# Kernel optimization log

Measured on AMD Instinct MI355X. Metric: run time of the kernel, lower is better.

The kernel has to match this reference:

```python
import jax, jax.numpy as jnp
import numpy as np

B, S, E = 2, 2048, 2048
H, KVH = 16, 4
HD = E // H          # 128
REP = H // KVH       # 4
THETA = 100000.0


def _rope_cos_sin(seqlen, head_dim, theta=THETA):
    # Faithful to precompute_pos_cis: exponent is arange(0, d, 2) (NOT divided by d)
    freqs = 1.0 / theta ** jnp.arange(0, head_dim, 2, dtype=jnp.float32)[: head_dim // 2]
    ang = jnp.outer(jnp.arange(seqlen, dtype=jnp.float32), freqs)  # (S, HD/2)
    return jnp.cos(ang), jnp.sin(ang)


def _apply_rotary(t, cos, sin):
    # t: (B, S, h, HD) -> complex pairs along last dim
    b, s, h, d = t.shape
    t = t.astype(jnp.float32).reshape(b, s, h, d // 2, 2)
    tr, ti = t[..., 0], t[..., 1]
    c = cos[None, :, None, :]
    sn = sin[None, :, None, :]
    out_r = tr * c - ti * sn
    out_i = tr * sn + ti * c
    return jnp.stack([out_r, out_i], axis=-1).reshape(b, s, h, d)


def setup_inputs() -> dict:
    key = jax.random.key(0)
    ks = jax.random.split(key, 9)
    sc_e = 1.0 / np.sqrt(E)
    return {
        "x": jax.random.normal(ks[0], (B, S, E), jnp.float32),
        "wq": jax.random.normal(ks[1], (E, H * HD), jnp.float32) * sc_e,
        "bq": jax.random.normal(ks[2], (H * HD,), jnp.float32) * 0.01,
        "wk": jax.random.normal(ks[3], (E, KVH * HD), jnp.float32) * sc_e,
        "bk": jax.random.normal(ks[4], (KVH * HD,), jnp.float32) * 0.01,
        "wv": jax.random.normal(ks[5], (E, KVH * HD), jnp.float32) * sc_e,
        "bv": jax.random.normal(ks[6], (KVH * HD,), jnp.float32) * 0.01,
        "wo": jax.random.normal(ks[7], (H * HD, E), jnp.float32) * sc_e,
        "bo": jax.random.normal(ks[8], (E,), jnp.float32) * 0.01,
    }


def reference(x, wq, bq, wk, bk, wv, bv, wo, bo):
    b, s, _ = x.shape
    xq = (x @ wq + bq).reshape(b, s, H, HD)
    xk = (x @ wk + bk).reshape(b, s, KVH, HD)
    xv = (x @ wv + bv).reshape(b, s, KVH, HD)

    cos, sin = _rope_cos_sin(s, HD)
    xq = _apply_rotary(xq, cos, sin)
    xk = _apply_rotary(xk, cos, sin)

    # GQA: group query heads over shared KV heads instead of materializing repeat_kv
    q = xq.transpose(0, 2, 1, 3).reshape(b, KVH, REP, s, HD)  # (B, G, R, S, D)
    k = xk.transpose(0, 2, 1, 3)                               # (B, G, S, D)
    v = xv.astype(jnp.float32).transpose(0, 2, 1, 3)           # (B, G, S, D)

    scores = jnp.einsum("bgrqd,bgkd->bgrqk", q, k) / jnp.sqrt(jnp.float32(HD))
    causal = jnp.tril(jnp.ones((s, s), dtype=bool))
    scores = jnp.where(causal[None, None, None], scores, jnp.float32(-jnp.inf))
    attn = jax.nn.softmax(scores, axis=-1)
    out = jnp.einsum("bgrqk,bgkd->bgrqd", attn, v)  # (B, G, R, S, D)
    out = out.reshape(b, H, s, HD).transpose(0, 2, 1, 3).reshape(b, s, H * HD)
    return out @ wo + bo
```

## Files before the change

### kernel.cpp

```cpp
#include <hip/hip_runtime.h>
#include <math.h>

#define BB 2
#define SS 2048
#define EE 2048
#define HH 16
#define KVH 4
#define HD 128

typedef __attribute__((ext_vector_type(8))) short short8;
typedef __attribute__((ext_vector_type(4))) float f32x4;

__device__ __forceinline__ short f2b(float f) {
  unsigned u = __float_as_uint(f);
  unsigned r = (u + 0x7fffu + ((u >> 16) & 1u)) >> 16;
  return (short)r;
}

__device__ __forceinline__ void async_load16(const void* g, void* l) {
  __builtin_amdgcn_global_load_lds(
      (const __attribute__((address_space(1))) void*)g,
      (__attribute__((address_space(3))) void*)l, 16, 0, 0);
}

__device__ __forceinline__ float rope_freq(int jp) {
  return exp2f(-(float)(2 * jp) * 16.609640474436812f);
}

__global__ void f32_to_bf16(const float* __restrict__ in, short* __restrict__ out) {
  int i = (blockIdx.x * 256 + threadIdx.x) * 8;
  float4 a = *(const float4*)(in + i);
  float4 b = *(const float4*)(in + i + 4);
  short8 c;
  c[0] = f2b(a.x); c[1] = f2b(a.y); c[2] = f2b(a.z); c[3] = f2b(a.w);
  c[4] = f2b(b.x); c[5] = f2b(b.y); c[6] = f2b(b.z); c[7] = f2b(b.w);
  *(short8*)(out + i) = c;
}

__global__ void transpose_f2b(const float* __restrict__ in, short* __restrict__ out,
                              int K, int N) {
  __shared__ short tile[32][33];
  int n0 = blockIdx.x * 32, k0 = blockIdx.y * 32;
  int tx = threadIdx.x, ty = threadIdx.y;
#pragma unroll
  for (int i = 0; i < 32; i += 8)
    tile[ty + i][tx] = f2b(in[(size_t)(k0 + ty + i) * N + n0 + tx]);
  __syncthreads();
#pragma unroll
  for (int i = 0; i < 32; i += 8)
    out[(size_t)(n0 + ty + i) * K + k0 + tx] = tile[tx][ty + i];
}

__global__ __launch_bounds__(256) void gemm_qkv(
    const short* __restrict__ A, const short* __restrict__ Bt,
    const float* __restrict__ bq, const float* __restrict__ bk,
    const float* __restrict__ bv,
    short* __restrict__ qbuf, short* __restrict__ kbuf, short* __restrict__ vtr) {
  __shared__ __align__(16) short Sm[128 * 136];
  short* Al = Sm;
  short* Bl = Sm + 128 * 64;
  const int K = EE;
  int t = threadIdx.x, lane = t & 63, w = t >> 6;
  int wm = (w >> 1) * 64, wn = (w & 1) * 64;
  int id = blockIdx.y * 32 + blockIdx.x;
  int swz = (id & 7) * 96 + (id >> 3);
  int m0 = (swz & 31) * 128, n0 = (swz >> 5) * 128;
  const short* Ab = A + (size_t)m0 * K;
  const short* Bb = Bt + (size_t)n0 * K;
  int srow = t >> 3, scol = (t & 7) * 8;
  int lj = lane & 15, lr = lane >> 4;
  f32x4 acc[4][4] = {};
  for (int k0 = 0; k0 < K; k0 += 64) {
#pragma unroll
    for (int q = 0; q < 4; q++) {
      async_load16(Ab + (size_t)(q * 32 + srow) * K + k0 + scol,
                   (char*)Al + q * 4096 + w * 1024);
      async_load16(Bb + (size_t)(q * 32 + srow) * K + k0 + scol,
                   (char*)Bl + q * 4096 + w * 1024);
    }
    __syncthreads();
    short8 a0[4], a1[4], b0[4], b1[4];
#pragma unroll
    for (int i = 0; i < 4; i++) {
      a0[i] = *(const short8*)&Al[(wm + i * 16 + lj) * 64 + lr * 8];
      a1[i] = *(const short8*)&Al[(wm + i * 16 + lj) * 64 + 32 + lr * 8];
    }
#pragma unroll
    for (int j = 0; j < 4; j++) {
      b0[j] = *(const short8*)&Bl[(wn + j * 16 + lj) * 64 + lr * 8];
      b1[j] = *(const short8*)&Bl[(wn + j * 16 + lj) * 64 + 32 + lr * 8];
    }
#pragma unroll
    for (int i = 0; i < 4; i++)
#pragma unroll
      for (int j = 0; j < 4; j++) {
        acc[i][j] = __builtin_amdgcn_mfma_f32_16x16x32_bf16(a0[i], b0[j], acc[i][j], 0, 0, 0);
        acc[i][j] = __builtin_amdgcn_mfma_f32_16x16x32_bf16(a1[i], b1[j], acc[i][j], 0, 0, 0);
      }
    __syncthreads();
  }
  if (n0 < 2048) {
#pragma unroll
    for (int j = 0; j < 4; j++) {
      int d = wn + j * 16 + lj;
      float bias = bq[n0 + d];
      float freq = rope_freq(d >> 1);
      bool odd = (d & 1) != 0;
#pragma unroll
      for (int i = 0; i < 4; i++)
#pragma unroll
        for (int r = 0; r < 4; r++) {
          int mloc = wm + i * 16 + lr * 4 + r;
          int s = (m0 + mloc) & (SS - 1);
          float val = acc[i][j][r] + bias;
          float other = __shfl_xor(val, 1, 64);
          float ang = (float)s * freq;
          float cs = cosf(ang), sn = sinf(ang);
          float res = odd ? (other * sn + val * cs) : (val * cs - other * sn);
          Sm[mloc * 136 + d] = f2b(res);
        }
    }
  } else if (n0 < 2560) {
    int base = n0 - 2048;
#pragma unroll
    for (int j = 0; j < 4; j++) {
      int d = wn + j * 16 + lj;
      float bias = bk[base + d];
      float freq = rope_freq(d >> 1);
      bool odd = (d & 1) != 0;
#pragma unroll
      for (int i = 0; i < 4; i++)
#pragma unroll
        for (int r = 0; r < 4; r++) {
          int mloc = wm + i * 16 + lr * 4 + r;
          int s = (m0 + mloc) & (SS - 1);
          float val = acc[i][j][r] + bias;
          float other = __shfl_xor(val, 1, 64);
          float ang = (float)s * freq;
          float cs = cosf(ang), sn = sinf(ang);
          float res = odd ? (other * sn + val * cs) : (val * cs - other * sn);
          Sm[mloc * 136 + d] = f2b(res);
        }
    }
  } else {
    int base = n0 - 2560;
#pragma unroll
    for (int j = 0; j < 4; j++) {
      int d = wn + j * 16 + lj;
      float bias = bv[base + d];
#pragma unroll
      for (int i = 0; i < 4; i++)
#pragma unroll
        for (int r = 0; r < 4; r++) {
          int mloc = wm + i * 16 + lr * 4 + r;
          Sm[d * 136 + mloc] = f2b(acc[i][j][r] + bias);
        }
    }
  }
  __syncthreads();
  int r0 = t >> 4, ch = t & 15;
  if (n0 < 2048) {
#pragma unroll
    for (int p = 0; p < 8; p++) {
      int row = p * 16 + r0;
      *(short8*)(qbuf + (size_t)(m0 + row) * 2048 + n0 + ch * 8) =
          *(const short8*)&Sm[row * 136 + ch * 8];
    }
  } else if (n0 < 2560) {
    int kvh = (n0 - 2048) >> 7;
    int b = m0 >> 11, s0 = m0 & (SS - 1);
    short* dst = kbuf + ((size_t)(b * KVH + kvh) * SS + s0) * HD;
#pragma unroll
    for (int p = 0; p < 8; p++) {
      int row = p * 16 + r0;
      *(short8*)(dst + (size_t)row * HD + ch * 8) = *(const short8*)&Sm[row * 136 + ch * 8];
    }
  } else {
    int kvh = (n0 - 2560) >> 7;
    int b = m0 >> 11, s0 = m0 & (SS - 1);
    short* dst = vtr + ((size_t)(b * KVH + kvh) * HD) * SS + s0;
#pragma unroll
    for (int p = 0; p < 8; p++) {
      int row = p * 16 + r0;
      *(short8*)(dst + (size_t)row * SS + ch * 8) = *(const short8*)&Sm[row * 136 + ch * 8];
    }
  }
}

__global__ __launch_bounds__(256) void attn_kernel(
    const short* __restrict__ qb, const short* __restrict__ kb,
    const short* __restrict__ vt, short* __restrict__ ao) {
  __shared__ __align__(16) short Kl[64 * 128];
  __shared__ __align__(16) short Vl[128 * 64];
  __shared__ __align__(16) short Pl[4 * 16 * 64];
  int t = threadIdx.x, lane = t & 63, w = t >> 6;
  int lj = lane & 15, lr = lane >> 4;
  int id = blockIdx.x + (blockIdx.y << 5) + (blockIdx.z << 9);
  int swz = (id & 7) * 128 + (id >> 3);
  int qt = swz & 31, h = (swz >> 5) & 15, b = swz >> 9;
  int kvh = h >> 2;
  int qb0 = qt * 64;
  const short* qbase = qb + (size_t)(b * SS) * 2048 + h * HD;
  const short* kbase = kb + (size_t)(b * KVH + kvh) * SS * HD;
  const short* vbase = vt + (size_t)(b * KVH + kvh) * HD * SS;
  short8 aq[4];
  int sq = qb0 + w * 16 + lj;
#pragma unroll
  for (int kk = 0; kk < 4; kk++)
    aq[kk] = *(const short8*)(qbase + (size_t)sq * 2048 + kk * 32 + lr * 8);
  f32x4 O[8] = {};
  const float NEG = -1e30f;
  float mrow[4] = {NEG, NEG, NEG, NEG};
  float lrow[4] = {0.f, 0.f, 0.f, 0.f};
  const float scale = 0.088388347648318447f;
  int nkt = qt + 1;
  for (int kt = 0; kt < nkt; ++kt) {
    short8 gk[4], gv[4];
#pragma unroll
    for (int i = 0; i < 4; i++) {
      gk[i] = *(const short8*)(kbase + (size_t)(kt * 64 + i * 16 + (t >> 4)) * HD + (t & 15) * 8);
      gv[i] = *(const short8*)(vbase + (size_t)(i * 32 + (t >> 3)) * SS + kt * 64 + (t & 7) * 8);
    }
#pragma unroll
    for (int i = 0; i < 4; i++) {
      *(short8*)&Kl[(i * 16 + (t >> 4)) * 128 + (t & 15) * 8] = gk[i];
      *(short8*)&Vl[(i * 32 + (t >> 3)) * 64 + (t & 7) * 8] = gv[i];
    }
    __syncthreads();
    f32x4 S[4];
#pragma unroll
    for (int nt = 0; nt < 4; nt++) {
      f32x4 sc = {};
#pragma unroll
      for (int kk = 0; kk < 4; kk++) {
        short8 bk_ = *(const short8*)&Kl[(nt * 16 + lj) * 128 + kk * 32 + lr * 8];
        sc = __builtin_amdgcn_mfma_f32_16x16x32_bf16(aq[kk], bk_, sc, 0, 0, 0);
      }
      S[nt] = sc;
    }
    int rowg = qb0 + w * 16 + lr * 4;
#pragma unroll
    for (int nt = 0; nt < 4; nt++) {
      int colg = kt * 64 + nt * 16 + lj;
#pragma unroll
      for (int r = 0; r < 4; r++) {
        float v = S[nt][r] * scale;
        if (colg > rowg + r) v = NEG;
        S[nt][r] = v;
      }
    }
    float alpha[4];
#pragma unroll
    for (int r = 0; r < 4; r++) {
      float m_ = fmaxf(fmaxf(S[0][r], S[1][r]), fmaxf(S[2][r], S[3][r]));
#pragma unroll
      for (int off = 1; off < 16; off <<= 1) m_ = fmaxf(m_, __shfl_xor(m_, off, 64));
      float mn = fmaxf(mrow[r], m_);
      alpha[r] = __expf(mrow[r] - mn);
      mrow[r] = mn;
    }
    float ls[4] = {0.f, 0.f, 0.f, 0.f};
#pragma unroll
    for (int nt = 0; nt < 4; nt++)
#pragma unroll
      for (int r = 0; r < 4; r++) {
        float p = __expf(S[nt][r] - mrow[r]);
        ls[r] += p;
        Pl[(w * 16 + lr * 4 + r) * 64 + nt * 16 + lj] = f2b(p);
      }
#pragma unroll
    for (int r = 0; r < 4; r++) {
      float s_ = ls[r];
#pragma unroll
      for (int off = 1; off < 16; off <<= 1) s_ += __shfl_xor(s_, off, 64);
      lrow[r] = lrow[r] * alpha[r] + s_;
    }
#pragma unroll
    for (int jt = 0; jt < 8; jt++)
#pragma unroll
      for (int r = 0; r < 4; r++) O[jt][r] *= alpha[r];
#pragma unroll
    for (int kk = 0; kk < 2; kk++) {
      short8 ap = *(const short8*)&Pl[(w * 16 + lj) * 64 + kk * 32 + lr * 8];
#pragma unroll
      for (int jt = 0; jt < 8; jt++) {
        short8 bv_ = *(const short8*)&Vl[(jt * 16 + lj) * 64 + kk * 32 + lr * 8];
        O[jt] = __builtin_amdgcn_mfma_f32_16x16x32_bf16(ap, bv_, O[jt], 0, 0, 0);
      }
    }
    __syncthreads();
  }
  size_t obase = (size_t)(b * SS + qb0 + w * 16) * 2048 + h * HD;
#pragma unroll
  for (int jt = 0; jt < 8; jt++)
#pragma unroll
    for (int r = 0; r < 4; r++) {
      int row = lr * 4 + r;
      ao[obase + (size_t)row * 2048 + jt * 16 + lj] = f2b(O[jt][r] / lrow[r]);
    }
}

__global__ __launch_bounds__(256) void gemm_out(
    const short* __restrict__ A, const short* __restrict__ Bt,
    const float* __restrict__ bo, float* __restrict__ out) {
  __shared__ __align__(16) short Al[128 * 32];
  __shared__ __align__(16) short Bl[128 * 32];
  const int K = EE;
  int t = threadIdx.x, lane = t & 63, w = t >> 6;
  int wm = (w >> 1) * 64, wn = (w & 1) * 64;
  int id = blockIdx.y * 32 + blockIdx.x;
  int swz = (id & 7) * 64 + (id >> 3);
  int m0 = (swz & 31) * 128, n0 = (swz >> 5) * 128;
  const short* Ab = A + (size_t)m0 * K;
  const short* Bb = Bt + (size_t)n0 * K;
  int sr = t >> 2, sc = (t & 3) * 8;
  char* AlB = (char*)Al + w * 1024;
  char* BlB = (char*)Bl + w * 1024;
  f32x4 acc[4][4] = {};
  for (int k0 = 0; k0 < K; k0 += 32) {
    async_load16(Ab + (size_t)sr * K + k0 + sc, AlB);
    async_load16(Ab + (size_t)(64 + sr) * K + k0 + sc, AlB + 4096);
    async_load16(Bb + (size_t)sr * K + k0 + sc, BlB);
    async_load16(Bb + (size_t)(64 + sr) * K + k0 + sc, BlB + 4096);
    __syncthreads();
    short8 a[4], b[4];
#pragma unroll
    for (int i = 0; i < 4; i++)
      a[i] = *(const short8*)&Al[(wm + i * 16 + (lane & 15)) * 32 + (lane >> 4) * 8];
#pragma unroll
    for (int j = 0; j < 4; j++)
      b[j] = *(const short8*)&Bl[(wn + j * 16 + (lane & 15)) * 32 + (lane >> 4) * 8];
#pragma unroll
    for (int i = 0; i < 4; i++)
#pragma unroll
      for (int j = 0; j < 4; j++)
        acc[i][j] = __builtin_amdgcn_mfma_f32_16x16x32_bf16(a[i], b[j], acc[i][j], 0, 0, 0);
    __syncthreads();
  }
#pragma unroll
  for (int j = 0; j < 4; j++) {
    int n = n0 + wn + j * 16 + (lane & 15);
    float bias = bo[n];
#pragma unroll
    for (int i = 0; i < 4; i++)
#pragma unroll
      for (int r = 0; r < 4; r++) {
        int m = m0 + wm + i * 16 + (lane >> 4) * 4 + r;
        out[(size_t)m * 2048 + n] = acc[i][j][r] + bias;
      }
  }
}

extern "C" void kernel_launch(void* const* d_in, const int* in_sizes, int n_in,
                              void* d_out, int out_size, void* d_ws, size_t ws_size,
                              hipStream_t stream) {
  const float* x  = (const float*)d_in[0];
  const float* wq = (const float*)d_in[1];
  const float* bq = (const float*)d_in[2];
  const float* wk = (const float*)d_in[3];
  const float* bk = (const float*)d_in[4];
  const float* wv = (const float*)d_in[5];
  const float* bv = (const float*)d_in[6];
  const float* wo = (const float*)d_in[7];
  const float* bo = (const float*)d_in[8];
  float* out = (float*)d_out;

  short* W1t = (short*)d_ws;
  short* Wot = W1t + (size_t)3072 * 2048;
  short* qb_ = Wot + (size_t)2048 * 2048;
  short* kb_ = qb_ + (size_t)4096 * 2048;
  short* vt_ = kb_ + (size_t)4096 * 512;
  short* ao_ = vt_ + (size_t)4096 * 512;
  short* xb_ = ao_;

  dim3 tb(32, 8);
  f32_to_bf16<<<4096, 256, 0, stream>>>(x, xb_);
  transpose_f2b<<<dim3(64, 64), tb, 0, stream>>>(wq, W1t, 2048, 2048);
  transpose_f2b<<<dim3(16, 64), tb, 0, stream>>>(wk, W1t + (size_t)2048 * 2048, 2048, 512);
  transpose_f2b<<<dim3(16, 64), tb, 0, stream>>>(wv, W1t + (size_t)2560 * 2048, 2048, 512);
  transpose_f2b<<<dim3(64, 64), tb, 0, stream>>>(wo, Wot, 2048, 2048);

  gemm_qkv<<<dim3(32, 24), 256, 0, stream>>>(xb_, W1t, bq, bk, bv, qb_, kb_, vt_);
  attn_kernel<<<dim3(32, 16, 2), 256, 0, stream>>>(qb_, kb_, vt_, ao_);
  gemm_out<<<dim3(32, 16), 256, 0, stream>>>(ao_, Wot, bo, out);
}
```

Before: 903.1 us.

## Retile QKV GEMM to 256x256 blocks with double-buffered async K-loads

The QKV projection GEMM moves from 128x128 tiles with 256 threads to 256x256 tiles with 512 threads. The K step drops to 32 and uses a double-buffered LDS pipeline, so the next slice is prefetched while MFMAs run on the current one. The epilogue is updated to handle 256-wide column tiles that span two heads. Larger tiles raise data reuse per block, but the grid shrinks to 192 blocks, fewer than the number of CUs, and the bigger LDS footprint limits occupancy.

```diff
diff --git a/kernel.cpp b/kernel.cpp
--- a/kernel.cpp
+++ b/kernel.cpp
@@ -51,138 +51,162 @@
     out[(size_t)(n0 + ty + i) * K + k0 + tx] = tile[tx][ty + i];
 }
 
-__global__ __launch_bounds__(256) void gemm_qkv(
+__global__ __launch_bounds__(512, 2) void gemm_qkv(
     const short* __restrict__ A, const short* __restrict__ Bt,
     const float* __restrict__ bq, const float* __restrict__ bk,
     const float* __restrict__ bv,
     short* __restrict__ qbuf, short* __restrict__ kbuf, short* __restrict__ vtr) {
-  __shared__ __align__(16) short Sm[128 * 136];
-  short* Al = Sm;
-  short* Bl = Sm + 128 * 64;
+  __shared__ __align__(16) short Sm[256 * 264];
   const int K = EE;
   int t = threadIdx.x, lane = t & 63, w = t >> 6;
-  int wm = (w >> 1) * 64, wn = (w & 1) * 64;
-  int id = blockIdx.y * 32 + blockIdx.x;
-  int swz = (id & 7) * 96 + (id >> 3);
-  int m0 = (swz & 31) * 128, n0 = (swz >> 5) * 128;
+  int lj = lane & 15, lr = lane >> 4;
+  int wm2 = (w >> 2) * 128, wn2 = (w & 3) * 64;
+  int m0 = blockIdx.x * 256, n0 = blockIdx.y * 256;
   const short* Ab = A + (size_t)m0 * K;
   const short* Bb = Bt + (size_t)n0 * K;
-  int srow = t >> 3, scol = (t & 7) * 8;
-  int lj = lane & 15, lr = lane >> 4;
-  f32x4 acc[4][4] = {};
-  for (int k0 = 0; k0 < K; k0 += 64) {
-#pragma unroll
-    for (int q = 0; q < 4; q++) {
-      async_load16(Ab + (size_t)(q * 32 + srow) * K + k0 + scol,
-                   (char*)Al + q * 4096 + w * 1024);
-      async_load16(Bb + (size_t)(q * 32 + srow) * K + k0 + scol,
-                   (char*)Bl + q * 4096 + w * 1024);
-    }
+  int srow = t >> 2, scol = (t & 3) * 8;
+  char* ldsA = (char*)Sm + w * 1024;
+  char* ldsB = (char*)Sm + 16384 + w * 1024;
+  f32x4 acc[8][4] = {};
+#pragma unroll
+  for (int q = 0; q < 2; q++) {
+    async_load16(Ab + (size_t)(q * 128 + srow) * K + scol, ldsA + q * 8192);
+    async_load16(Bb + (size_t)(q * 128 + srow) * K + scol, ldsB + q * 8192);
+  }
+  __syncthreads();
+  int cur = 0;
+  for (int kt = 0; kt < 63; kt++) {
+    int nxt = cur ^ 1;
+    int k0 = (kt + 1) * 32;
+#pragma unroll
+    for (int q = 0; q < 2; q++) {
+      async_load16(Ab + (size_t)(q * 128 + srow) * K + k0 + scol,
+                   ldsA + nxt * 32768 + q * 8192);
+      async_load16(Bb + (size_t)(q * 128 + srow) * K + k0 + scol,
+                   ldsB + nxt * 32768 + q * 8192);
+    }
+    const short* Ac = Sm + cur * 16384;
+    const short* Bc = Sm + cur * 16384 + 8192;
+    short8 a[8], b[4];
+#pragma unroll
+    for (int i = 0; i < 8; i++)
+      a[i] = *(const short8*)&Ac[(wm2 + i * 16 + lj) * 32 + lr * 8];
+#pragma unroll
+    for (int j = 0; j < 4; j++)
+      b[j] = *(const short8*)&Bc[(wn2 + j * 16 + lj) * 32 + lr * 8];
+#pragma unroll
+    for (int i = 0; i < 8; i++)
+#pragma unroll
+      for (int j = 0; j < 4; j++)
+        acc[i][j] = __builtin_amdgcn_mfma_f32_16x16x32_bf16(a[i], b[j], acc[i][j], 0, 0, 0);
     __syncthreads();
-    short8 a0[4], a1[4], b0[4], b1[4];
-#pragma unroll
-    for (int i = 0; i < 4; i++) {
-      a0[i] = *(const short8*)&Al[(wm + i * 16 + lj) * 64 + lr * 8];
-      a1[i] = *(const short8*)&Al[(wm + i * 16 + lj) * 64 + 32 + lr * 8];
-    }
+    cur = nxt;
+  }
+  {
+    const short* Ac = Sm + cur * 16384;
+    const short* Bc = Sm + cur * 16384 + 8192;
+    short8 a[8], b[4];
+#pragma unroll
+    for (int i = 0; i < 8; i++)
+      a[i] = *(const short8*)&Ac[(wm2 + i * 16 + lj) * 32 + lr * 8];
+#pragma unroll
+    for (int j = 0; j < 4; j++)
+      b[j] = *(const short8*)&Bc[(wn2 + j * 16 + lj) * 32 + lr * 8];
+#pragma unroll
+    for (int i = 0; i < 8; i++)
+#pragma unroll
+      for (int j = 0; j < 4; j++)
+        acc[i][j] = __builtin_amdgcn_mfma_f32_16x16x32_bf16(a[i], b[j], acc[i][j], 0, 0, 0);
+  }
+  __syncthreads();
+  if (n0 < 2048) {
 #pragma unroll
     for (int j = 0; j < 4; j++) {
-      b0[j] = *(const short8*)&Bl[(wn + j * 16 + lj) * 64 + lr * 8];
-      b1[j] = *(const short8*)&Bl[(wn + j * 16 + lj) * 64 + 32 + lr * 8];
-    }
-#pragma unroll
-    for (int i = 0; i < 4; i++)
-#pragma unroll
-      for (int j = 0; j < 4; j++) {
-        acc[i][j] = __builtin_amdgcn_mfma_f32_16x16x32_bf16(a0[i], b0[j], acc[i][j], 0, 0, 0);
-        acc[i][j] = __builtin_amdgcn_mfma_f32_16x16x32_bf16(a1[i], b1[j], acc[i][j], 0, 0, 0);
-      }
-    __syncthreads();
-  }
-  if (n0 < 2048) {
-#pragma unroll
-    for (int j = 0; j < 4; j++) {
-      int d = wn + j * 16 + lj;
-      float bias = bq[n0 + d];
-      float freq = rope_freq(d >> 1);
-      bool odd = (d & 1) != 0;
-#pragma unroll
-      for (int i = 0; i < 4; i++)
+      int dl = wn2 + j * 16 + lj;
+      float bias = bq[n0 + dl];
+      float freq = rope_freq((dl & 127) >> 1);
+      bool odd = (dl & 1) != 0;
+#pragma unroll
+      for (int i = 0; i < 8; i++)
 #pragma unroll
         for (int r = 0; r < 4; r++) {
-          int mloc = wm + i * 16 + lr * 4 + r;
+          int mloc = wm2 + i * 16 + lr * 4 + r;
           int s = (m0 + mloc) & (SS - 1);
           float val = acc[i][j][r] + bias;
           float other = __shfl_xor(val, 1, 64);
           float ang = (float)s * freq;
           float cs = cosf(ang), sn = sinf(ang);
           float res = odd ? (other * sn + val * cs) : (val * cs - other * sn);
-          Sm[mloc * 136 + d] = f2b(res);
+          Sm[mloc * 264 + dl] = f2b(res);
         }
     }
   } else if (n0 < 2560) {
     int base = n0 - 2048;
 #pragma unroll
     for (int j = 0; j < 4; j++) {
-      int d = wn + j * 16 + lj;
-      float bias = bk[base + d];
-      float freq = rope_freq(d >> 1);
-      bool odd = (d & 1) != 0;
-#pragma unroll
-      for (int i = 0; i < 4; i++)
+      int dl = wn2 + j * 16 + lj;
+      float bias = bk[base + dl];
+      float freq = rope_freq((dl & 127) >> 1);
+      bool odd = (dl & 1) != 0;
+#pragma unroll
+      for (int i = 0; i < 8; i++)
 #pragma unroll
         for (int r = 0; r < 4; r++) {
-          int mloc = wm + i * 16 + lr * 4 + r;
+          int mloc = wm2 + i * 16 + lr * 4 + r;
           int s = (m0 + mloc) & (SS - 1);
           float val = acc[i][j][r] + bias;
           float other = __shfl_xor(val, 1, 64);
           float ang = (float)s * freq;
           float cs = cosf(ang), sn = sinf(ang);
           float res = odd ? (other * sn + val * cs) : (val * cs - other * sn);
-          Sm[mloc * 136 + d] = f2b(res);
+          Sm[mloc * 264 + dl] = f2b(res);
         }
     }
   } else {
     int base = n0 - 2560;
 #pragma unroll
     for (int j = 0; j < 4; j++) {
-      int d = wn + j * 16 + lj;
-      float bias = bv[base + d];
-#pragma unroll
-      for (int i = 0; i < 4; i++)
+      int dl = wn2 + j * 16 + lj;
+      float bias = bv[base + dl];
+#pragma unroll
+      for (int i = 0; i < 8; i++)
 #pragma unroll
         for (int r = 0; r < 4; r++) {
-          int mloc = wm + i * 16 + lr * 4 + r;
-          Sm[d * 136 + mloc] = f2b(acc[i][j][r] + bias);
+          int mloc = wm2 + i * 16 + lr * 4 + r;
+          Sm[dl * 264 + mloc] = f2b(acc[i][j][r] + bias);
         }
     }
   }
   __syncthreads();
-  int r0 = t >> 4, ch = t & 15;
+  int r0 = t >> 5, ch = t & 31;
   if (n0 < 2048) {
 #pragma unroll
-    for (int p = 0; p < 8; p++) {
+    for (int p = 0; p < 16; p++) {
       int row = p * 16 + r0;
       *(short8*)(qbuf + (size_t)(m0 + row) * 2048 + n0 + ch * 8) =
-          *(const short8*)&Sm[row * 136 + ch * 8];
+          *(const short8*)&Sm[row * 264 + ch * 8];
     }
   } else if (n0 < 2560) {
-    int kvh = (n0 - 2048) >> 7;
-    int b = m0 >> 11, s0 = m0 & (SS - 1);
-    short* dst = kbuf + ((size_t)(b * KVH + kvh) * SS + s0) * HD;
-#pragma unroll
-    for (int p = 0; p < 8; p++) {
+    int base = n0 - 2048;
+    int bb = m0 >> 11, s0 = m0 & (SS - 1);
+    int col = base + ch * 8;
+    int kvh = col >> 7, d = col & 127;
+    short* dst = kbuf + ((size_t)(bb * KVH + kvh) * SS + s0) * HD + d;
+#pragma unroll
+    for (int p = 0; p < 16; p++) {
       int row = p * 16 + r0;
-      *(short8*)(dst + (size_t)row * HD + ch * 8) = *(const short8*)&Sm[row * 136 + ch * 8];
+      *(short8*)(dst + (size_t)row * HD) = *(const short8*)&Sm[row * 264 + ch * 8];
     }
   } else {
-    int kvh = (n0 - 2560) >> 7;
-    int b = m0 >> 11, s0 = m0 & (SS - 1);
-    short* dst = vtr + ((size_t)(b * KVH + kvh) * HD) * SS + s0;
-#pragma unroll
-    for (int p = 0; p < 8; p++) {
-      int row = p * 16 + r0;
-      *(short8*)(dst + (size_t)row * SS + ch * 8) = *(const short8*)&Sm[row * 136 + ch * 8];
+    int base = n0 - 2560;
+    int bb = m0 >> 11, s0 = m0 & (SS - 1);
+#pragma unroll
+    for (int p = 0; p < 16; p++) {
+      int dl = p * 16 + r0;
+      int col = base + dl;
+      int kvh = col >> 7, d = col & 127;
+      *(short8*)(vtr + ((size_t)(bb * KVH + kvh) * HD + d) * SS + s0 + ch * 8) =
+          *(const short8*)&Sm[dl * 264 + ch * 8];
     }
   }
 }
@@ -380,7 +404,7 @@
   transpose_f2b<<<dim3(16, 64), tb, 0, stream>>>(wv, W1t + (size_t)2560 * 2048, 2048, 512);
   transpose_f2b<<<dim3(64, 64), tb, 0, stream>>>(wo, Wot, 2048, 2048);
 
-  gemm_qkv<<<dim3(32, 24), 256, 0, stream>>>(xb_, W1t, bq, bk, bv, qb_, kb_, vt_);
+  gemm_qkv<<<dim3(16, 12), 512, 0, stream>>>(xb_, W1t, bq, bk, bv, qb_, kb_, vt_);
   attn_kernel<<<dim3(32, 16, 2), 256, 0, stream>>>(qb_, kb_, vt_, ao_);
   gemm_out<<<dim3(32, 16), 256, 0, stream>>>(ao_, Wot, bo, out);
 }
```

Result: slower. 1.751 ms (+93.8%).

## Enlarge GEMM block tiles to 256x128 with 512 threads

Applied to the files above, without the earlier changes.

Both the QKV projection GEMM and the output GEMM now use 512-thread blocks, each covering a 256x128 output tile. The output GEMM also moves from a K-step of 32 to 64. Larger tiles halve the number of blocks and raise reuse of each loaded B tile, while the longer K-step halves the number of barriers in the output GEMM. The block-ID swizzle for L2 locality is dropped, and the grids drop to 384 and 256 blocks, which may leave compute units underfilled. The QKV epilogue rewrite, including the RoPE section that is not shown, must be consistent with the new LDS strides, and that part is unclear.

```diff
diff --git a/kernel.cpp b/kernel.cpp
--- a/kernel.cpp
+++ b/kernel.cpp
@@ -51,39 +51,37 @@
     out[(size_t)(n0 + ty + i) * K + k0 + tx] = tile[tx][ty + i];
 }
 
-__global__ __launch_bounds__(256) void gemm_qkv(
+__global__ __launch_bounds__(512, 4) void gemm_qkv(
     const short* __restrict__ A, const short* __restrict__ Bt,
     const float* __restrict__ bq, const float* __restrict__ bk,
     const float* __restrict__ bv,
     short* __restrict__ qbuf, short* __restrict__ kbuf, short* __restrict__ vtr) {
-  __shared__ __align__(16) short Sm[128 * 136];
-  short* Al = Sm;
-  short* Bl = Sm + 128 * 64;
+  __shared__ __align__(16) short Sm[256 * 136];
+  short* Bl = Sm + 16384;
   const int K = EE;
   int t = threadIdx.x, lane = t & 63, w = t >> 6;
+  int lj = lane & 15, lr = lane >> 4;
   int wm = (w >> 1) * 64, wn = (w & 1) * 64;
-  int id = blockIdx.y * 32 + blockIdx.x;
-  int swz = (id & 7) * 96 + (id >> 3);
-  int m0 = (swz & 31) * 128, n0 = (swz >> 5) * 128;
+  int m0 = blockIdx.x * 256, n0 = blockIdx.y * 128;
   const short* Ab = A + (size_t)m0 * K;
   const short* Bb = Bt + (size_t)n0 * K;
   int srow = t >> 3, scol = (t & 7) * 8;
-  int lj = lane & 15, lr = lane >> 4;
+  char* ldsA = (char*)Sm + w * 1024;
+  char* ldsB = (char*)Sm + 32768 + w * 1024;
   f32x4 acc[4][4] = {};
   for (int k0 = 0; k0 < K; k0 += 64) {
 #pragma unroll
-    for (int q = 0; q < 4; q++) {
-      async_load16(Ab + (size_t)(q * 32 + srow) * K + k0 + scol,
-                   (char*)Al + q * 4096 + w * 1024);
-      async_load16(Bb + (size_t)(q * 32 + srow) * K + k0 + scol,
-                   (char*)Bl + q * 4096 + w * 1024);
-    }
+    for (int q = 0; q < 4; q++)
+      async_load16(Ab + (size_t)(q * 64 + srow) * K + k0 + scol, ldsA + q * 8192);
+#pragma unroll
+    for (int q = 0; q < 2; q++)
+      async_load16(Bb + (size_t)(q * 64 + srow) * K + k0 + scol, ldsB + q * 8192);
     __syncthreads();
     short8 a0[4], a1[4], b0[4], b1[4];
 #pragma unroll
     for (int i = 0; i < 4; i++) {
-      a0[i] = *(const short8*)&Al[(wm + i * 16 + lj) * 64 + lr * 8];
-      a1[i] = *(const short8*)&Al[(wm + i * 16 + lj) * 64 + 32 + lr * 8];
+      a0[i] = *(const short8*)&Sm[(wm + i * 16 + lj) * 64 + lr * 8];
+      a1[i] = *(const short8*)&Sm[(wm + i * 16 + lj) * 64 + 32 + lr * 8];
     }
 #pragma unroll
     for (int j = 0; j < 4; j++) {
@@ -153,36 +151,38 @@
 #pragma unroll
         for (int r = 0; r < 4; r++) {
           int mloc = wm + i * 16 + lr * 4 + r;
-          Sm[d * 136 + mloc] = f2b(acc[i][j][r] + bias);
+          Sm[d * 264 + mloc] = f2b(acc[i][j][r] + bias);
         }
     }
   }
   __syncthreads();
-  int r0 = t >> 4, ch = t & 15;
   if (n0 < 2048) {
+    int r0 = t >> 4, ch = t & 15;
 #pragma unroll
     for (int p = 0; p < 8; p++) {
-      int row = p * 16 + r0;
+      int row = p * 32 + r0;
       *(short8*)(qbuf + (size_t)(m0 + row) * 2048 + n0 + ch * 8) =
           *(const short8*)&Sm[row * 136 + ch * 8];
     }
   } else if (n0 < 2560) {
+    int r0 = t >> 4, ch = t & 15;
     int kvh = (n0 - 2048) >> 7;
     int b = m0 >> 11, s0 = m0 & (SS - 1);
     short* dst = kbuf + ((size_t)(b * KVH + kvh) * SS + s0) * HD;
 #pragma unroll
     for (int p = 0; p < 8; p++) {
-      int row = p * 16 + r0;
+      int row = p * 32 + r0;
       *(short8*)(dst + (size_t)row * HD + ch * 8) = *(const short8*)&Sm[row * 136 + ch * 8];
     }
   } else {
+    int r0 = t >> 5, ch = t & 31;
     int kvh = (n0 - 2560) >> 7;
     int b = m0 >> 11, s0 = m0 & (SS - 1);
     short* dst = vtr + ((size_t)(b * KVH + kvh) * HD) * SS + s0;
 #pragma unroll
     for (int p = 0; p < 8; p++) {
-      int row = p * 16 + r0;
-      *(short8*)(dst + (size_t)row * SS + ch * 8) = *(const short8*)&Sm[row * 136 + ch * 8];
+      int dl = p * 16 + r0;
+      *(short8*)(dst + (size_t)dl * SS + ch * 8) = *(const short8*)&Sm[dl * 264 + ch * 8];
     }
   }
 }
@@ -300,52 +300,59 @@
     }
 }
 
-__global__ __launch_bounds__(256) void gemm_out(
+__global__ __launch_bounds__(512, 4) void gemm_out(
     const short* __restrict__ A, const short* __restrict__ Bt,
     const float* __restrict__ bo, float* __restrict__ out) {
-  __shared__ __align__(16) short Al[128 * 32];
-  __shared__ __align__(16) short Bl[128 * 32];
+  __shared__ __align__(16) short Sm[24576];
+  short* Bl = Sm + 16384;
   const int K = EE;
   int t = threadIdx.x, lane = t & 63, w = t >> 6;
+  int lj = lane & 15, lr = lane >> 4;
   int wm = (w >> 1) * 64, wn = (w & 1) * 64;
-  int id = blockIdx.y * 32 + blockIdx.x;
-  int swz = (id & 7) * 64 + (id >> 3);
-  int m0 = (swz & 31) * 128, n0 = (swz >> 5) * 128;
+  int m0 = blockIdx.x * 256, n0 = blockIdx.y * 128;
   const short* Ab = A + (size_t)m0 * K;
   const short* Bb = Bt + (size_t)n0 * K;
-  int sr = t >> 2, sc = (t & 3) * 8;
-  char* AlB = (char*)Al + w * 1024;
-  char* BlB = (char*)Bl + w * 1024;
+  int srow = t >> 3, scol = (t & 7) * 8;
+  char* ldsA = (char*)Sm + w * 1024;
+  char* ldsB = (char*)Sm + 32768 + w * 1024;
   f32x4 acc[4][4] = {};
-  for (int k0 = 0; k0 < K; k0 += 32) {
-    async_load16(Ab + (size_t)sr * K + k0 + sc, AlB);
-    async_load16(Ab + (size_t)(64 + sr) * K + k0 + sc, AlB + 4096);
-    async_load16(Bb + (size_t)sr * K + k0 + sc, BlB);
-    async_load16(Bb + (size_t)(64 + sr) * K + k0 + sc, BlB + 4096);
-    __syncthreads();
-    short8 a[4], b[4];
+  for (int k0 = 0; k0 < K; k0 += 64) {
+#pragma unroll
+    for (int q = 0; q < 4; q++)
+      async_load16(Ab + (size_t)(q * 64 + srow) * K + k0 + scol, ldsA + q * 8192);
+#pragma unroll
+    for (int q = 0; q < 2; q++)
+      async_load16(Bb + (size_t)(q * 64 + srow) * K + k0 + scol, ldsB + q * 8192);
+    __syncthreads();
+    short8 a0[4], a1[4], b0[4], b1[4];
+#pragma unroll
+    for (int i = 0; i < 4; i++) {
+      a0[i] = *(const short8*)&Sm[(wm + i * 16 + lj) * 64 + lr * 8];
+      a1[i] = *(const short8*)&Sm[(wm + i * 16 + lj) * 64 + 32 + lr * 8];
+    }
+#pragma unroll
+    for (int j = 0; j < 4; j++) {
+      b0[j] = *(const short8*)&Bl[(wn + j * 16 + lj) * 64 + lr * 8];
+      b1[j] = *(const short8*)&Bl[(wn + j * 16 + lj) * 64 + 32 + lr * 8];
+    }
 #pragma unroll
     for (int i = 0; i < 4; i++)
-      a[i] = *(const short8*)&Al[(wm + i * 16 + (lane & 15)) * 32 + (lane >> 4) * 8];
-#pragma unroll
-    for (int j = 0; j < 4; j++)
-      b[j] = *(const short8*)&Bl[(wn + j * 16 + (lane & 15)) * 32 + (lane >> 4) * 8];
+#pragma unroll
+      for (int j = 0; j < 4; j++) {
+        acc[i][j] = __builtin_amdgcn_mfma_f32_16x16x32_bf16(a0[i], b0[j], acc[i][j], 0, 0, 0);
+        acc[i][j] = __builtin_amdgcn_mfma_f32_16x16x32_bf16(a1[i], b1[j], acc[i][j], 0, 0, 0);
+      }
+    __syncthreads();
+  }
+#pragma unroll
+  for (int j = 0; j < 4; j++) {
+    int n = n0 + wn + j * 16 + lj;
+    float bias = bo[n];
 #pragma unroll
     for (int i = 0; i < 4; i++)
 #pragma unroll
-      for (int j = 0; j < 4; j++)
-        acc[i][j] = __builtin_amdgcn_mfma_f32_16x16x32_bf16(a[i], b[j], acc[i][j], 0, 0, 0);
-    __syncthreads();
-  }
-#pragma unroll
-  for (int j = 0; j < 4; j++) {
-    int n = n0 + wn + j * 16 + (lane & 15);
-    float bias = bo[n];
-#pragma unroll
-    for (int i = 0; i < 4; i++)
-#pragma unroll
       for (int r = 0; r < 4; r++) {
-        int m = m0 + wm + i * 16 + (lane >> 4) * 4 + r;
+        int m = m0 + wm + i * 16 + lr * 4 + r;
         out[(size_t)m * 2048 + n] = acc[i][j][r] + bias;
       }
   }
@@ -380,7 +387,7 @@
   transpose_f2b<<<dim3(16, 64), tb, 0, stream>>>(wv, W1t + (size_t)2560 * 2048, 2048, 512);
   transpose_f2b<<<dim3(64, 64), tb, 0, stream>>>(wo, Wot, 2048, 2048);
 
-  gemm_qkv<<<dim3(32, 24), 256, 0, stream>>>(xb_, W1t, bq, bk, bv, qb_, kb_, vt_);
+  gemm_qkv<<<dim3(16, 24), 512, 0, stream>>>(xb_, W1t, bq, bk, bv, qb_, kb_, vt_);
   attn_kernel<<<dim3(32, 16, 2), 256, 0, stream>>>(qb_, kb_, vt_, ao_);
-  gemm_out<<<dim3(32, 16), 256, 0, stream>>>(ao_, Wot, bo, out);
-}
+  gemm_out<<<dim3(16, 16), 512, 0, stream>>>(ao_, Wot, bo, out);
+}
```

New measurement: 982.8 us. +8.8%, slower.
